# Optimization experiments

Hardware: AMD Instinct MI355X
Metric: run time of the kernel (lower is better)

## Reference

```python
import jax, jax.numpy as jnp
import numpy as np

N, L, D = 2048, 200, 64
NUM_USERS, NUM_ITEMS, NUM_R = 100000, 100000, 5


def _lin(x, W, b):
    # torch nn.Linear convention: W is [out, in]
    return x @ W.T + b


def setup_inputs() -> dict:
    key = jax.random.key(0)
    ks = jax.random.split(key, 12)
    s = 0.05
    return dict(
        nodes=jax.random.randint(ks[0], (N,), 0, NUM_ITEMS),
        history_uv=jax.random.randint(ks[1], (N, L), 0, NUM_USERS),
        history_r=jax.random.randint(ks[2], (N, L), 0, NUM_R),
        u2e=jax.random.normal(ks[3], (NUM_USERS, D), dtype=jnp.float32) * s,
        v2e=jax.random.normal(ks[4], (NUM_ITEMS, D), dtype=jnp.float32) * s,
        r2e=jax.random.normal(ks[5], (NUM_R, D), dtype=jnp.float32) * s,
        w_r1_w=jax.random.normal(ks[6], (D, 2 * D), dtype=jnp.float32) * s,
        w_r1_b=jnp.zeros((D,), jnp.float32),
        w_r2_w=jax.random.normal(ks[7], (D, D), dtype=jnp.float32) * s,
        w_r2_b=jnp.zeros((D,), jnp.float32),
        mu_w=jax.random.normal(ks[8], (D, 2 * D), dtype=jnp.float32) * s,
        mu_b=jnp.zeros((D,), jnp.float32),
        att1_w=jax.random.normal(ks[9], (D, 2 * D), dtype=jnp.float32) * s,
        att1_b=jnp.zeros((D,), jnp.float32),
        att2_w=jax.random.normal(ks[10], (D, D), dtype=jnp.float32) * s,
        att2_b=jnp.zeros((D,), jnp.float32),
        att3_w=jax.random.normal(ks[11], (1, D), dtype=jnp.float32) * s,
        att3_b=jnp.zeros((1,), jnp.float32),
    )


def reference(nodes, history_uv, history_r, u2e, v2e, r2e,
              w_r1_w, w_r1_b, w_r2_w, w_r2_b, mu_w, mu_b,
              att1_w, att1_b, att2_w, att2_b, att3_w, att3_b):
    # uv=False branch: neighbors are users, center nodes are items
    e_uv = u2e[history_uv]                     # [N, L, D]
    q = v2e[nodes]                             # [N, D]
    e_r = r2e[history_r]                       # [N, L, D]

    x = jax.nn.relu(_lin(jnp.concatenate([e_uv, e_r], -1), w_r1_w, w_r1_b))
    o = jax.nn.relu(_lin(x, w_r2_w, w_r2_b))   # [N, L, D]

    qb = jnp.broadcast_to(q[:, None, :], o.shape)   # [N, L, D]
    g = jax.nn.sigmoid(_lin(jnp.concatenate([o, qb], -1), mu_w, mu_b))
    o = g * o + (1.0 - g) * qb                 # gated history rep

    # Attention (dropout disabled / eval mode), softmax over the L neighbors
    a = jax.nn.relu(_lin(jnp.concatenate([o, qb], -1), att1_w, att1_b))
    a = jax.nn.relu(_lin(a, att2_w, att2_b))
    a = _lin(a, att3_w, att3_b)                # [N, L, 1]
    w = jax.nn.softmax(a, axis=1)

    return jnp.sum(w * o, axis=1)              # [N, D]
```

## Files before the change

### kernel.cpp

```cpp
#include <hip/hip_runtime.h>
#include <hip/hip_bf16.h>

typedef float f32x4 __attribute__((ext_vector_type(4)));
typedef __bf16 bf16x8 __attribute__((ext_vector_type(8)));

union Frag { unsigned short h[8]; unsigned int u[4]; uint4 u4; bf16x8 b; };

__device__ __forceinline__ unsigned short f2bs(float f){
  __hip_bfloat16 v = __float2bfloat16(f);
  return __builtin_bit_cast(unsigned short, v);
}
__device__ __forceinline__ unsigned int pk2(float a, float b){
  unsigned int r;
  asm("v_cvt_pk_bf16_f32 %0, %1, %2" : "=v"(r) : "v"(a), "v"(b));
  return r;
}
__device__ __forceinline__ Frag packF(f32x4 a, f32x4 b){
  Frag f;
  f.u[0] = pk2(a[0], a[1]); f.u[1] = pk2(a[2], a[3]);
  f.u[2] = pk2(b[0], b[1]); f.u[3] = pk2(b[2], b[3]);
  return f;
}
__device__ __forceinline__ f32x4 relu4(f32x4 v){
  f32x4 r;
  #pragma unroll
  for (int j = 0; j < 4; ++j) r[j] = fmaxf(v[j], 0.f);
  return r;
}
__device__ __forceinline__ float sigmoid_fast(float x){
  return __builtin_amdgcn_rcpf(1.f + __expf(-x));
}

__global__ void prep_weights(const float* __restrict__ w1, const float* __restrict__ w2,
                             const float* __restrict__ mu, const float* __restrict__ a1,
                             const float* __restrict__ a2, const float* __restrict__ r2e,
                             const float* __restrict__ b1, uint4* __restrict__ ws){
  const int f = blockIdx.x;
  const int l = threadIdx.x;
  Frag fr;
  if (f < 64){
    const float* W; int m, s, K;
    if (f < 16)      { W = w1; m = f >> 2;        s = f & 3;        K = 128; }
    else if (f < 24) { W = w2; m = (f - 16) >> 1; s = (f - 16) & 1; K = 64;  }
    else if (f < 40) { W = mu; m = (f - 24) >> 2; s = (f - 24) & 3; K = 128; }
    else if (f < 56) { W = a1; m = (f - 40) >> 2; s = (f - 40) & 3; K = 128; }
    else             { W = a2; m = (f - 56) >> 1; s = (f - 56) & 1; K = 64;  }
    const int row = 16 * m + (l & 15);
    const int k0  = 32 * s + 4 * (l >> 4);
    #pragma unroll
    for (int h = 0; h < 2; ++h)
      #pragma unroll
      for (int j = 0; j < 4; ++j)
        fr.h[4*h + j] = f2bs(W[row * K + k0 + 16*h + j]);
    ws[f * 64 + l] = fr.u4;
  } else if (f < 74){
    const int f2 = f - 64;
    const int R = f2 >> 1, sp = f2 & 1;
    const int g = (l >> 4) & 3;
    #pragma unroll
    for (int h = 0; h < 2; ++h)
      #pragma unroll
      for (int j = 0; j < 4; ++j)
        fr.h[4*h + j] = f2bs(r2e[R * 64 + sp * 32 + 16*h + 4*g + j]);
    ws[4096 + f2 * 64 + l] = fr.u4;
  } else {
    float* r1c = (float*)(ws + 4736);
    const int d = l;
    for (int R = 0; R < 5; ++R){
      float s = b1[d];
      for (int k = 0; k < 64; ++k)
        s = fmaf(w1[d * 128 + 64 + k], r2e[R * 64 + k], s);
      r1c[R * 68 + d] = s;
    }
  }
}

__global__ __launch_bounds__(256)
void uv_agg_main(const int* __restrict__ nodes, const int* __restrict__ huv,
                 const int* __restrict__ hr, const float* __restrict__ u2e,
                 const float* __restrict__ v2e,
                 const float* __restrict__ b1g, const float* __restrict__ b2g,
                 const float* __restrict__ bmg, const float* __restrict__ ba1g,
                 const float* __restrict__ ba2g, const float* __restrict__ a3g,
                 const uint4* __restrict__ wsfrag, float* __restrict__ out){
  extern __shared__ unsigned char smem[];
  uint4* wlds = (uint4*)smem;
  float* bias = (float*)(smem + 65536);
  float* r1cl = (float*)(smem + 67072);

  const int tid  = threadIdx.x;
  const int lane = tid & 63;
  const int wave = tid >> 6;
  const int g    = lane >> 4;
  const int r16  = lane & 15;
  const int n    = blockIdx.x * 4 + wave;

  #pragma unroll 4
  for (int i = tid; i < 4096; i += 256) wlds[i] = wsfrag[i];
  for (int i = tid; i < 384; i += 256){
    const int w = i >> 6, d = i & 63;
    const float* src = (w==0)?b1g:(w==1)?b2g:(w==2)?bmg:(w==3)?ba1g:(w==4)?ba2g:a3g;
    bias[i] = src[d];
  }
  {
    const float* r1g = (const float*)(wsfrag + 4736);
    for (int i = tid; i < 340; i += 256) r1cl[i] = r1g[i];
  }
  __syncthreads();

  const uint4* wl = wlds + lane;
  const f32x4* bl = (const f32x4*)bias + g;
  const int* hu  = huv + n * 200;
  const int* hrw = hr  + n * 200;

  const int item = nodes[n];
  f32x4 qv[4];
  #pragma unroll
  for (int m = 0; m < 4; ++m)
    qv[m] = *(const f32x4*)(v2e + (size_t)item * 64 + 16*m + 4*g);
  Frag qf[2];
  qf[0] = packF(qv[0], qv[1]); qf[1] = packF(qv[2], qv[3]);

  f32x4 muq[4], a1q[4];
  #pragma unroll
  for (int m = 0; m < 4; ++m){
    f32x4 a = bl[2*16 + 4*m];
    {
      Frag w; w.u4 = wl[(24 + m*4 + 2) * 64];
      a = __builtin_amdgcn_mfma_f32_16x16x32_bf16(w.b, qf[0].b, a, 0, 0, 0);
      w.u4 = wl[(24 + m*4 + 3) * 64];
      a = __builtin_amdgcn_mfma_f32_16x16x32_bf16(w.b, qf[1].b, a, 0, 0, 0);
    }
    muq[m] = a;
    f32x4 b = bl[3*16 + 4*m];
    {
      Frag w; w.u4 = wl[(40 + m*4 + 2) * 64];
      b = __builtin_amdgcn_mfma_f32_16x16x32_bf16(w.b, qf[0].b, b, 0, 0, 0);
      w.u4 = wl[(40 + m*4 + 3) * 64];
      b = __builtin_amdgcn_mfma_f32_16x16x32_bf16(w.b, qf[1].b, b, 0, 0, 0);
    }
    a1q[m] = b;
  }

  float swl = 0.f;
  f32x4 accw[4];
  #pragma unroll
  for (int m = 0; m < 4; ++m) accw[m] = (f32x4)(0.f);

  int irA, irB;
  f32x4 urA[4], urB[4];
  {
    const int iuA = hu[r16];      irA = hrw[r16];
    const int iuB = hu[16 + r16]; irB = hrw[16 + r16];
    const f32x4* ua = (const f32x4*)(u2e + (size_t)iuA * 64);
    const f32x4* ub = (const f32x4*)(u2e + (size_t)iuB * 64);
    #pragma unroll
    for (int s = 0; s < 4; ++s){ urA[s] = ua[4*s + g]; urB[s] = ub[4*s + g]; }
  }

  for (int it = 0; it < 7; ++it){
    Frag b0A[2], b0B[2];
    b0A[0] = packF(urA[0], urA[1]); b0A[1] = packF(urA[2], urA[3]);
    b0B[0] = packF(urB[0], urB[1]); b0B[1] = packF(urB[2], urB[3]);
    const int ircA = irA, ircB = irB;
    const bool vA = (it < 6) || (r16 < 8);
    const bool vB = (it < 6);

    if (it < 6){
      const int base = 32*it + 32;
      const int kA = min(base + r16, 199);
      const int kB = min(base + 16 + r16, 199);
      const int iuA = hu[kA]; irA = hrw[kA];
      const int iuB = hu[kB]; irB = hrw[kB];
      const f32x4* ua = (const f32x4*)(u2e + (size_t)iuA * 64);
      const f32x4* ub = (const f32x4*)(u2e + (size_t)iuB * 64);
      #pragma unroll
      for (int s = 0; s < 4; ++s){ urA[s] = ua[4*s + g]; urB[s] = ub[4*s + g]; }
    }

    f32x4 XA[4], XB[4];
    __builtin_amdgcn_s_setprio(1);
    #pragma unroll
    for (int m = 0; m < 4; ++m){
      f32x4 aA = *(const f32x4*)&r1cl[ircA*68 + 16*m + 4*g];
      f32x4 aB = *(const f32x4*)&r1cl[ircB*68 + 16*m + 4*g];
      #pragma unroll
      for (int s = 0; s < 2; ++s){
        Frag w; w.u4 = wl[(m*4 + s) * 64];
        aA = __builtin_amdgcn_mfma_f32_16x16x32_bf16(w.b, b0A[s].b, aA, 0, 0, 0);
        aB = __builtin_amdgcn_mfma_f32_16x16x32_bf16(w.b, b0B[s].b, aB, 0, 0, 0);
      }
      XA[m] = relu4(aA); XB[m] = relu4(aB);
    }
    __builtin_amdgcn_s_setprio(0);
    Frag bxA[2], bxB[2];
    bxA[0] = packF(XA[0], XA[1]); bxA[1] = packF(XA[2], XA[3]);
    bxB[0] = packF(XB[0], XB[1]); bxB[1] = packF(XB[2], XB[3]);

    f32x4 OA[4], OB[4];
    __builtin_amdgcn_s_setprio(1);
    #pragma unroll
    for (int m = 0; m < 4; ++m){
      const f32x4 bi = bl[1*16 + 4*m];
      f32x4 aA = bi, aB = bi;
      #pragma unroll
      for (int s = 0; s < 2; ++s){
        Frag w; w.u4 = wl[(16 + m*2 + s) * 64];
        aA = __builtin_amdgcn_mfma_f32_16x16x32_bf16(w.b, bxA[s].b, aA, 0, 0, 0);
        aB = __builtin_amdgcn_mfma_f32_16x16x32_bf16(w.b, bxB[s].b, aB, 0, 0, 0);
      }
      OA[m] = relu4(aA); OB[m] = relu4(aB);
    }
    __builtin_amdgcn_s_setprio(0);
    Frag boA[2], boB[2];
    boA[0] = packF(OA[0], OA[1]); boA[1] = packF(OA[2], OA[3]);
    boB[0] = packF(OB[0], OB[1]); boB[1] = packF(OB[2], OB[3]);

    f32x4 OGA[4], OGB[4];
    __builtin_amdgcn_s_setprio(1);
    #pragma unroll
    for (int m = 0; m < 4; ++m){
      f32x4 aA = muq[m], aB = muq[m];
      #pragma unroll
      for (int s = 0; s < 2; ++s){
        Frag w; w.u4 = wl[(24 + m*4 + s) * 64];
        aA = __builtin_amdgcn_mfma_f32_16x16x32_bf16(w.b, boA[s].b, aA, 0, 0, 0);
        aB = __builtin_amdgcn_mfma_f32_16x16x32_bf16(w.b, boB[s].b, aB, 0, 0, 0);
      }
      #pragma unroll
      for (int j = 0; j < 4; ++j){
        const float gA = sigmoid_fast(aA[j]);
        const float gB = sigmoid_fast(aB[j]);
        OGA[m][j] = fmaf(gA, OA[m][j] - qv[m][j], qv[m][j]);
        OGB[m][j] = fmaf(gB, OB[m][j] - qv[m][j], qv[m][j]);
      }
    }
    __builtin_amdgcn_s_setprio(0);
    Frag bgA[2], bgB[2];
    bgA[0] = packF(OGA[0], OGA[1]); bgA[1] = packF(OGA[2], OGA[3]);
    bgB[0] = packF(OGB[0], OGB[1]); bgB[1] = packF(OGB[2], OGB[3]);

    f32x4 A1A[4], A1B[4];
    __builtin_amdgcn_s_setprio(1);
    #pragma unroll
    for (int m = 0; m < 4; ++m){
      f32x4 aA = a1q[m], aB = a1q[m];
      #pragma unroll
      for (int s = 0; s < 2; ++s){
        Frag w; w.u4 = wl[(40 + m*4 + s) * 64];
        aA = __builtin_amdgcn_mfma_f32_16x16x32_bf16(w.b, bgA[s].b, aA, 0, 0, 0);
        aB = __builtin_amdgcn_mfma_f32_16x16x32_bf16(w.b, bgB[s].b, aB, 0, 0, 0);
      }
      A1A[m] = relu4(aA); A1B[m] = relu4(aB);
    }
    __builtin_amdgcn_s_setprio(0);
    Frag b4A[2], b4B[2];
    b4A[0] = packF(A1A[0], A1A[1]); b4A[1] = packF(A1A[2], A1A[3]);
    b4B[0] = packF(A1B[0], A1B[1]); b4B[1] = packF(A1B[2], A1B[3]);

    float pA = 0.f, pB = 0.f;
    __builtin_amdgcn_s_setprio(1);
    #pragma unroll
    for (int m = 0; m < 4; ++m){
      const f32x4 bi = bl[4*16 + 4*m];
      f32x4 aA = bi, aB = bi;
      #pragma unroll
      for (int s = 0; s < 2; ++s){
        Frag w; w.u4 = wl[(56 + m*2 + s) * 64];
        aA = __builtin_amdgcn_mfma_f32_16x16x32_bf16(w.b, b4A[s].b, aA, 0, 0, 0);
        aB = __builtin_amdgcn_mfma_f32_16x16x32_bf16(w.b, b4B[s].b, aB, 0, 0, 0);
      }
      aA = relu4(aA); aB = relu4(aB);
      const f32x4 a3m = bl[5*16 + 4*m];
      #pragma unroll
      for (int j = 0; j < 4; ++j){
        pA = fmaf(a3m[j], aA[j], pA);
        pB = fmaf(a3m[j], aB[j], pB);
      }
    }
    __builtin_amdgcn_s_setprio(0);
    pA += __shfl_xor(pA, 16); pA += __shfl_xor(pA, 32);
    pB += __shfl_xor(pB, 16); pB += __shfl_xor(pB, 32);

    const float eA = vA ? __expf(fminf(pA, 60.f)) : 0.f;
    const float eB = vB ? __expf(fminf(pB, 60.f)) : 0.f;
    swl += eA + eB;
    #pragma unroll
    for (int m = 0; m < 4; ++m)
      #pragma unroll
      for (int j = 0; j < 4; ++j)
        accw[m][j] = fmaf(eA, OGA[m][j], fmaf(eB, OGB[m][j], accw[m][j]));
  }

  #pragma unroll
  for (int o = 1; o < 16; o <<= 1){
    #pragma unroll
    for (int m = 0; m < 4; ++m)
      #pragma unroll
      for (int j = 0; j < 4; ++j)
        accw[m][j] += __shfl_xor(accw[m][j], o);
    swl += __shfl_xor(swl, o);
  }
  if (r16 == 0){
    const float inv = 1.f / swl;
    #pragma unroll
    for (int m = 0; m < 4; ++m){
      f32x4 v = accw[m];
      #pragma unroll
      for (int j = 0; j < 4; ++j) v[j] *= inv;
      *(f32x4*)(out + (size_t)n * 64 + 16*m + 4*g) = v;
    }
  }
}

extern "C" void kernel_launch(void* const* d_in, const int* in_sizes, int n_in,
                              void* d_out, int out_size, void* d_ws, size_t ws_size,
                              hipStream_t stream){
  const int*   nodes = (const int*)  d_in[0];
  const int*   huv   = (const int*)  d_in[1];
  const int*   hr    = (const int*)  d_in[2];
  const float* u2e   = (const float*)d_in[3];
  const float* v2e   = (const float*)d_in[4];
  const float* r2e   = (const float*)d_in[5];
  const float* w1    = (const float*)d_in[6];
  const float* b1    = (const float*)d_in[7];
  const float* w2    = (const float*)d_in[8];
  const float* b2    = (const float*)d_in[9];
  const float* muw   = (const float*)d_in[10];
  const float* mub   = (const float*)d_in[11];
  const float* a1w   = (const float*)d_in[12];
  const float* a1b   = (const float*)d_in[13];
  const float* a2w   = (const float*)d_in[14];
  const float* a2b   = (const float*)d_in[15];
  const float* a3w   = (const float*)d_in[16];

  const int N = in_sizes[0];
  uint4* ws = (uint4*)d_ws;

  hipLaunchKernelGGL(prep_weights, dim3(75), dim3(64), 0, stream,
                     w1, w2, muw, a1w, a2w, r2e, b1, ws);
  hipLaunchKernelGGL(uv_agg_main, dim3(N / 4), dim3(256), 68432, stream,
                     nodes, huv, hr, u2e, v2e,
                     b1, b2, mub, a1b, a2b, a3w,
                     (const uint4*)ws, (float*)d_out);
}
```

Measured before the change: 48.10 us.

## Split each node's neighbor loop across two waves and trim LDS weight fragments

Each block now processes two nodes with two waves per node, each wave handling about half of the 13 neighbor tiles, and the partial softmax numerators and denominators are merged through shared memory. Unused weight fragments (the r2e half of w1 and the q-side halves of mu/att1) are removed from the LDS copy, shrinking shared memory per block, and the q-side fragments are read directly from global memory. This is meant to raise parallelism and occupancy, at the cost of more blocks each reloading weights and an extra block barrier plus reduction.

```diff
diff --git a/kernel.cpp b/kernel.cpp
--- a/kernel.cpp
+++ b/kernel.cpp
@@ -37,34 +37,26 @@
                              const float* __restrict__ b1, uint4* __restrict__ ws){
   const int f = blockIdx.x;
   const int l = threadIdx.x;
-  Frag fr;
-  if (f < 64){
+  if (f < 56){
     const float* W; int m, s, K;
-    if (f < 16)      { W = w1; m = f >> 2;        s = f & 3;        K = 128; }
-    else if (f < 24) { W = w2; m = (f - 16) >> 1; s = (f - 16) & 1; K = 64;  }
-    else if (f < 40) { W = mu; m = (f - 24) >> 2; s = (f - 24) & 3; K = 128; }
-    else if (f < 56) { W = a1; m = (f - 40) >> 2; s = (f - 40) & 3; K = 128; }
-    else             { W = a2; m = (f - 56) >> 1; s = (f - 56) & 1; K = 64;  }
+    if (f < 8)       { W = w1; m = f >> 1;        s = f & 1;            K = 128; }
+    else if (f < 16) { W = w2; m = (f - 8) >> 1;  s = (f - 8) & 1;      K = 64;  }
+    else if (f < 24) { W = mu; m = (f - 16) >> 1; s = (f - 16) & 1;     K = 128; }
+    else if (f < 32) { W = a1; m = (f - 24) >> 1; s = (f - 24) & 1;     K = 128; }
+    else if (f < 40) { W = a2; m = (f - 32) >> 1; s = (f - 32) & 1;     K = 64;  }
+    else if (f < 48) { W = mu; m = (f - 40) >> 1; s = 2 + ((f - 40) & 1); K = 128; }
+    else             { W = a1; m = (f - 48) >> 1; s = 2 + ((f - 48) & 1); K = 128; }
     const int row = 16 * m + (l & 15);
     const int k0  = 32 * s + 4 * (l >> 4);
+    Frag fr;
     #pragma unroll
     for (int h = 0; h < 2; ++h)
       #pragma unroll
       for (int j = 0; j < 4; ++j)
         fr.h[4*h + j] = f2bs(W[row * K + k0 + 16*h + j]);
     ws[f * 64 + l] = fr.u4;
-  } else if (f < 74){
-    const int f2 = f - 64;
-    const int R = f2 >> 1, sp = f2 & 1;
-    const int g = (l >> 4) & 3;
-    #pragma unroll
-    for (int h = 0; h < 2; ++h)
-      #pragma unroll
-      for (int j = 0; j < 4; ++j)
-        fr.h[4*h + j] = f2bs(r2e[R * 64 + sp * 32 + 16*h + 4*g + j]);
-    ws[4096 + f2 * 64 + l] = fr.u4;
   } else {
-    float* r1c = (float*)(ws + 4736);
+    float* r1c = (float*)(ws + 3584);
     const int d = l;
     for (int R = 0; R < 5; ++R){
       float s = b1[d];
@@ -85,25 +77,29 @@
                  const uint4* __restrict__ wsfrag, float* __restrict__ out){
   extern __shared__ unsigned char smem[];
   uint4* wlds = (uint4*)smem;
-  float* bias = (float*)(smem + 65536);
-  float* r1cl = (float*)(smem + 67072);
+  float* bias = (float*)(smem + 40960);
+  float* r1cl = (float*)(smem + 42496);
+  float* mAcc = (float*)(smem + 43856);
+  float* mSw  = (float*)(smem + 44880);
 
   const int tid  = threadIdx.x;
   const int lane = tid & 63;
   const int wave = tid >> 6;
+  const int ns   = wave >> 1;
+  const int half = wave & 1;
   const int g    = lane >> 4;
   const int r16  = lane & 15;
-  const int n    = blockIdx.x * 4 + wave;
-
-  #pragma unroll 4
-  for (int i = tid; i < 4096; i += 256) wlds[i] = wsfrag[i];
+  const int n    = blockIdx.x * 2 + ns;
+
+  #pragma unroll
+  for (int i = tid; i < 2560; i += 256) wlds[i] = wsfrag[i];
   for (int i = tid; i < 384; i += 256){
     const int w = i >> 6, d = i & 63;
     const float* src = (w==0)?b1g:(w==1)?b2g:(w==2)?bmg:(w==3)?ba1g:(w==4)?ba2g:a3g;
     bias[i] = src[d];
   }
   {
-    const float* r1g = (const float*)(wsfrag + 4736);
+    const float* r1g = (const float*)(wsfrag + 3584);
     for (int i = tid; i < 340; i += 256) r1cl[i] = r1g[i];
   }
   __syncthreads();
@@ -126,17 +122,17 @@
   for (int m = 0; m < 4; ++m){
     f32x4 a = bl[2*16 + 4*m];
     {
-      Frag w; w.u4 = wl[(24 + m*4 + 2) * 64];
+      Frag w; w.u4 = wsfrag[(40 + m*2 + 0) * 64 + lane];
       a = __builtin_amdgcn_mfma_f32_16x16x32_bf16(w.b, qf[0].b, a, 0, 0, 0);
-      w.u4 = wl[(24 + m*4 + 3) * 64];
+      w.u4 = wsfrag[(40 + m*2 + 1) * 64 + lane];
       a = __builtin_amdgcn_mfma_f32_16x16x32_bf16(w.b, qf[1].b, a, 0, 0, 0);
     }
     muq[m] = a;
     f32x4 b = bl[3*16 + 4*m];
     {
-      Frag w; w.u4 = wl[(40 + m*4 + 2) * 64];
+      Frag w; w.u4 = wsfrag[(48 + m*2 + 0) * 64 + lane];
       b = __builtin_amdgcn_mfma_f32_16x16x32_bf16(w.b, qf[0].b, b, 0, 0, 0);
-      w.u4 = wl[(40 + m*4 + 3) * 64];
+      w.u4 = wsfrag[(48 + m*2 + 1) * 64 + lane];
       b = __builtin_amdgcn_mfma_f32_16x16x32_bf16(w.b, qf[1].b, b, 0, 0, 0);
     }
     a1q[m] = b;
@@ -146,30 +142,38 @@
   f32x4 accw[4];
   #pragma unroll
   for (int m = 0; m < 4; ++m) accw[m] = (f32x4)(0.f);
+
+  const int nIt = half ? 3 : 4;
+  const int t0  = half ? 7 : 0;
 
   int irA, irB;
   f32x4 urA[4], urB[4];
   {
-    const int iuA = hu[r16];      irA = hrw[r16];
-    const int iuB = hu[16 + r16]; irB = hrw[16 + r16];
+    const int kA = min(16*t0 + r16, 199);
+    const int kB = min(16*t0 + 16 + r16, 199);
+    const int iuA = hu[kA]; irA = hrw[kA];
+    const int iuB = hu[kB]; irB = hrw[kB];
     const f32x4* ua = (const f32x4*)(u2e + (size_t)iuA * 64);
     const f32x4* ub = (const f32x4*)(u2e + (size_t)iuB * 64);
     #pragma unroll
     for (int s = 0; s < 4; ++s){ urA[s] = ua[4*s + g]; urB[s] = ub[4*s + g]; }
   }
 
-  for (int it = 0; it < 7; ++it){
+  for (int it = 0; it < nIt; ++it){
+    const int tA = t0 + 2*it;
+    const int tB = (half == 0 && it == 3) ? 13 : (t0 + 2*it + 1);
     Frag b0A[2], b0B[2];
     b0A[0] = packF(urA[0], urA[1]); b0A[1] = packF(urA[2], urA[3]);
     b0B[0] = packF(urB[0], urB[1]); b0B[1] = packF(urB[2], urB[3]);
     const int ircA = irA, ircB = irB;
-    const bool vA = (it < 6) || (r16 < 8);
-    const bool vB = (it < 6);
-
-    if (it < 6){
-      const int base = 32*it + 32;
-      const int kA = min(base + r16, 199);
-      const int kB = min(base + 16 + r16, 199);
+    const bool vA = (16*tA + r16) < 200;
+    const bool vB = (16*tB + r16) < 200;
+
+    if (it + 1 < nIt){
+      const int tAn = t0 + 2*it + 2;
+      const int tBn = (half == 0 && it + 1 == 3) ? 13 : (t0 + 2*it + 3);
+      const int kA = min(16*tAn + r16, 199);
+      const int kB = min(16*tBn + r16, 199);
       const int iuA = hu[kA]; irA = hrw[kA];
       const int iuB = hu[kB]; irB = hrw[kB];
       const f32x4* ua = (const f32x4*)(u2e + (size_t)iuA * 64);
@@ -186,7 +190,7 @@
       f32x4 aB = *(const f32x4*)&r1cl[ircB*68 + 16*m + 4*g];
       #pragma unroll
       for (int s = 0; s < 2; ++s){
-        Frag w; w.u4 = wl[(m*4 + s) * 64];
+        Frag w; w.u4 = wl[(m*2 + s) * 64];
         aA = __builtin_amdgcn_mfma_f32_16x16x32_bf16(w.b, b0A[s].b, aA, 0, 0, 0);
         aB = __builtin_amdgcn_mfma_f32_16x16x32_bf16(w.b, b0B[s].b, aB, 0, 0, 0);
       }
@@ -205,7 +209,7 @@
       f32x4 aA = bi, aB = bi;
       #pragma unroll
       for (int s = 0; s < 2; ++s){
-        Frag w; w.u4 = wl[(16 + m*2 + s) * 64];
+        Frag w; w.u4 = wl[(8 + m*2 + s) * 64];
         aA = __builtin_amdgcn_mfma_f32_16x16x32_bf16(w.b, bxA[s].b, aA, 0, 0, 0);
         aB = __builtin_amdgcn_mfma_f32_16x16x32_bf16(w.b, bxB[s].b, aB, 0, 0, 0);
       }
@@ -223,7 +227,7 @@
       f32x4 aA = muq[m], aB = muq[m];
       #pragma unroll
       for (int s = 0; s < 2; ++s){
-        Frag w; w.u4 = wl[(24 + m*4 + s) * 64];
+        Frag w; w.u4 = wl[(16 + m*2 + s) * 64];
         aA = __builtin_amdgcn_mfma_f32_16x16x32_bf16(w.b, boA[s].b, aA, 0, 0, 0);
         aB = __builtin_amdgcn_mfma_f32_16x16x32_bf16(w.b, boB[s].b, aB, 0, 0, 0);
       }
@@ -247,7 +251,7 @@
       f32x4 aA = a1q[m], aB = a1q[m];
       #pragma unroll
       for (int s = 0; s < 2; ++s){
-        Frag w; w.u4 = wl[(40 + m*4 + s) * 64];
+        Frag w; w.u4 = wl[(24 + m*2 + s) * 64];
         aA = __builtin_amdgcn_mfma_f32_16x16x32_bf16(w.b, bgA[s].b, aA, 0, 0, 0);
         aB = __builtin_amdgcn_mfma_f32_16x16x32_bf16(w.b, bgB[s].b, aB, 0, 0, 0);
       }
@@ -266,7 +270,7 @@
       f32x4 aA = bi, aB = bi;
       #pragma unroll
       for (int s = 0; s < 2; ++s){
-        Frag w; w.u4 = wl[(56 + m*2 + s) * 64];
+        Frag w; w.u4 = wl[(32 + m*2 + s) * 64];
         aA = __builtin_amdgcn_mfma_f32_16x16x32_bf16(w.b, b4A[s].b, aA, 0, 0, 0);
         aB = __builtin_amdgcn_mfma_f32_16x16x32_bf16(w.b, b4B[s].b, aB, 0, 0, 0);
       }
@@ -302,14 +306,18 @@
     swl += __shfl_xor(swl, o);
   }
   if (r16 == 0){
-    const float inv = 1.f / swl;
-    #pragma unroll
-    for (int m = 0; m < 4; ++m){
-      f32x4 v = accw[m];
-      #pragma unroll
-      for (int j = 0; j < 4; ++j) v[j] *= inv;
-      *(f32x4*)(out + (size_t)n * 64 + 16*m + 4*g) = v;
-    }
+    float* dst = mAcc + (ns * 2 + half) * 64;
+    #pragma unroll
+    for (int m = 0; m < 4; ++m)
+      *(f32x4*)(dst + 16*m + 4*g) = accw[m];
+    if (lane == 0) mSw[ns * 2 + half] = swl;
+  }
+  __syncthreads();
+  if (tid < 128){
+    const int n2 = tid >> 6, d = tid & 63;
+    const float tot = mSw[n2 * 2] + mSw[n2 * 2 + 1];
+    const float v = (mAcc[n2 * 128 + d] + mAcc[n2 * 128 + 64 + d]) / tot;
+    out[(size_t)(blockIdx.x * 2 + n2) * 64 + d] = v;
   }
 }
 
@@ -337,9 +345,9 @@
   const int N = in_sizes[0];
   uint4* ws = (uint4*)d_ws;
 
-  hipLaunchKernelGGL(prep_weights, dim3(75), dim3(64), 0, stream,
+  hipLaunchKernelGGL(prep_weights, dim3(57), dim3(64), 0, stream,
                      w1, w2, muw, a1w, a2w, r2e, b1, ws);
-  hipLaunchKernelGGL(uv_agg_main, dim3(N / 4), dim3(256), 68432, stream,
+  hipLaunchKernelGGL(uv_agg_main, dim3(N / 2), dim3(256), 44896, stream,
                      nodes, huv, hr, u2e, v2e,
                      b1, b2, mub, a1b, a2b, a3w,
                      (const uint4*)ws, (float*)d_out);
```

After: 59.39 us. 23.5% more time.
